# Optimization experiments

Measured on AMD Instinct MI355X. Metric: run time of the kernel, lower is better.

Reference implementation:

```python
import jax, jax.numpy as jnp
import numpy as np

B, S, D = 64, 2048, 64  # (batch*heads, seq_len, head_dim)

def setup_inputs() -> dict:
    key = jax.random.key(0)
    kq, kk, kv = jax.random.split(key, 3)
    q = jax.random.normal(kq, (B, S, D), dtype=jnp.float32)
    k = jax.random.normal(kk, (B, S, D), dtype=jnp.float32)
    v = jax.random.normal(kv, (B, S, D), dtype=jnp.float32)
    return {"q": q, "k": k, "v": v}

def reference(q, k, v):
    # scores: [B, S, S] = q @ k^T (no scaling, matching the source module)
    scores = jnp.einsum('bqd,bkd->bqk', q, k)
    attn = jax.nn.softmax(scores, axis=-1)
    # dropout p=0.0 -> identity
    out = jnp.einsum('bqk,bkd->bqd', attn, v)
    return out
```

## Files before the change

### kernel.cpp

```cpp
#include <hip/hip_runtime.h>

typedef __attribute__((ext_vector_type(8))) __bf16 bf16x8;
typedef __attribute__((ext_vector_type(8))) _Float16 f16x8;
typedef __attribute__((ext_vector_type(4))) float f32x4;
typedef __attribute__((ext_vector_type(8))) unsigned short u16x8;
typedef __attribute__((ext_vector_type(2))) unsigned int u32x2;

#define SDIM 2048
#define DDIM 64
#define NBATCH 64
#define LOG2E 1.44269504088896340736f

#if __has_builtin(__builtin_amdgcn_exp2f)
#define EXP2F __builtin_amdgcn_exp2f
#else
#define EXP2F exp2f
#endif

__device__ inline unsigned short f2bf(float f) {
  unsigned u = __builtin_bit_cast(unsigned, f);
  u += 0x7fffu + ((u >> 16) & 1u);
  return (unsigned short)(u >> 16);
}
__device__ inline unsigned short f2h(float f) {
  return __builtin_bit_cast(unsigned short, (_Float16)f);
}

__device__ inline void gload_lds16(const void* g, void* l) {
  __builtin_amdgcn_global_load_lds(
      (const __attribute__((address_space(1))) unsigned int*)g,
      (__attribute__((address_space(3))) unsigned int*)l, 16, 0, 0);
}

__global__ __launch_bounds__(256) void prep_kernel(
    const float* __restrict__ k, const float* __restrict__ v,
    unsigned short* __restrict__ khf, unsigned short* __restrict__ vtb) {
  __shared__ float tile[64][65];
  const int b = blockIdx.x >> 5;
  const int s0 = (blockIdx.x & 31) * 64;
  const size_t base = ((size_t)b * SDIM + s0) * DDIM;

  {
    const float* src = k + base + threadIdx.x * 16;
    f32x4 a = *(const f32x4*)src;
    f32x4 b4 = *(const f32x4*)(src + 4);
    f32x4 c4 = *(const f32x4*)(src + 8);
    f32x4 d4 = *(const f32x4*)(src + 12);
    u16x8 o0, o1;
#pragma unroll
    for (int j = 0; j < 4; ++j) {
      o0[j] = f2h(a[j] * LOG2E);
      o0[4 + j] = f2h(b4[j] * LOG2E);
      o1[j] = f2h(c4[j] * LOG2E);
      o1[4 + j] = f2h(d4[j] * LOG2E);
    }
    unsigned short* dst = khf + base + threadIdx.x * 16;
    *(u16x8*)dst = o0;
    *(u16x8*)(dst + 8) = o1;
  }

  {
    int row = threadIdx.x >> 2;
    int c16 = (threadIdx.x & 3) * 16;
    const float* src = v + base + (size_t)row * DDIM + c16;
#pragma unroll
    for (int c = 0; c < 4; ++c) {
      f32x4 f = *(const f32x4*)(src + 4 * c);
      tile[row][c16 + 4 * c + 0] = f[0];
      tile[row][c16 + 4 * c + 1] = f[1];
      tile[row][c16 + 4 * c + 2] = f[2];
      tile[row][c16 + 4 * c + 3] = f[3];
    }
    __syncthreads();
    int d = threadIdx.x >> 2;
    int sc = (threadIdx.x & 3) * 16;
    u16x8 a, c;
#pragma unroll
    for (int j = 0; j < 8; ++j) a[j] = f2bf(tile[sc + j][d]);
#pragma unroll
    for (int j = 0; j < 8; ++j) c[j] = f2bf(tile[sc + 8 + j][d]);
    unsigned short* dst = vtb + ((size_t)b * DDIM + d) * SDIM + s0 + sc;
    *(u16x8*)dst = a;
    *(u16x8*)(dst + 8) = c;
  }
}

__global__ __launch_bounds__(256, 2) void attn_kernel(
    const float* __restrict__ q, const unsigned short* __restrict__ khf,
    const unsigned short* __restrict__ vt, float* __restrict__ out) {
  __shared__ __align__(16) unsigned short kv[2 * 16 * 512];
  __shared__ __align__(16) unsigned short pf[4 * 8 * 512];

  const int bid = blockIdx.x;
  const int b = (bid & 7) * 8 + (bid >> 6);
  const int qt = (bid >> 3) & 7;
  const int tid = threadIdx.x;
  const int w = tid >> 6;
  const int L = tid & 63;
  const int l15 = L & 15;
  const int l4 = L >> 4;

  const size_t boff = (size_t)b * (SDIM * DDIM);
  const int qg = qt * 256 + w * 64;

  f16x8 qb[4][2];
#pragma unroll
  for (int t = 0; t < 4; ++t)
#pragma unroll
    for (int c = 0; c < 2; ++c) {
      const float* src = q + boff + (size_t)(qg + t * 16 + l15) * DDIM + c * 32 + l4 * 8;
      f32x4 f0 = *(const f32x4*)(src);
      f32x4 f1 = *(const f32x4*)(src + 4);
      f16x8 h;
#pragma unroll
      for (int j = 0; j < 4; ++j) {
        h[j] = (_Float16)f0[j];
        h[4 + j] = (_Float16)f1[j];
      }
      qb[t][c] = h;
    }

  const int pwoff = (l15 + 16 * (l4 >> 1)) * 8 + 4 * (l4 & 1);
  unsigned short* pwave = pf + w * 4096;

  const unsigned short* gsrc[4];
  int gadv;
  if (w < 2) {
#pragma unroll
    for (int ff = 0; ff < 4; ++ff) {
      int f = w * 4 + ff;
      gsrc[ff] = khf + boff + (size_t)((f >> 1) * 16 + l15) * DDIM + (f & 1) * 32 + l4 * 8;
    }
    gadv = 64 * DDIM;
  } else {
#pragma unroll
    for (int ff = 0; ff < 4; ++ff) {
      int fg = (w - 2) * 4 + ff;
      gsrc[ff] = vt + boff + (size_t)((fg >> 1) * 16 + l15) * SDIM + (fg & 1) * 32 + l4 * 8;
    }
    gadv = 64;
  }
  const int fdbase = w * 4;

  f32x4 o[4][4];
  float lsum[4];
#pragma unroll
  for (int t = 0; t < 4; ++t) {
#pragma unroll
    for (int n = 0; n < 4; ++n) o[t][n] = (f32x4){0.f, 0.f, 0.f, 0.f};
    lsum[t] = 0.f;
  }

#pragma unroll
  for (int ff = 0; ff < 4; ++ff) gload_lds16(gsrc[ff], &kv[(fdbase + ff) * 512]);
#pragma unroll
  for (int ff = 0; ff < 4; ++ff) gsrc[ff] += gadv;

  for (int it = 0; it < SDIM / 64; ++it) {
    const int cur = it & 1;
    __syncthreads();
    if (it + 1 < SDIM / 64) {
#pragma unroll
      for (int ff = 0; ff < 4; ++ff)
        gload_lds16(gsrc[ff], &kv[(1 - cur) * 8192 + (fdbase + ff) * 512]);
#pragma unroll
      for (int ff = 0; ff < 4; ++ff) gsrc[ff] += gadv;
    }
    const unsigned short* kvc = &kv[cur * 8192];

#pragma unroll
    for (int nt = 0; nt < 4; ++nt) {
      f16x8 k0 = *(const f16x8*)&kvc[(nt * 2 + 0) * 512 + L * 8];
      f16x8 k1 = *(const f16x8*)&kvc[(nt * 2 + 1) * 512 + L * 8];
      const int pbase = (nt >> 1) * 512 + pwoff + (nt & 1) * 256;
#pragma unroll
      for (int t = 0; t < 4; ++t) {
        f32x4 acc = (f32x4){0.f, 0.f, 0.f, 0.f};
        acc = __builtin_amdgcn_mfma_f32_16x16x32_f16(k0, qb[t][0], acc, 0, 0, 0);
        acc = __builtin_amdgcn_mfma_f32_16x16x32_f16(k1, qb[t][1], acc, 0, 0, 0);
        float p0 = EXP2F(acc[0]), p1 = EXP2F(acc[1]);
        float p2 = EXP2F(acc[2]), p3 = EXP2F(acc[3]);
        lsum[t] += (p0 + p1) + (p2 + p3);
        unsigned a0 = __builtin_bit_cast(unsigned, p0) + 0x8000u;
        unsigned a1 = __builtin_bit_cast(unsigned, p1) + 0x8000u;
        unsigned a2 = __builtin_bit_cast(unsigned, p2) + 0x8000u;
        unsigned a3 = __builtin_bit_cast(unsigned, p3) + 0x8000u;
        u32x2 wv;
        wv[0] = __builtin_amdgcn_perm(a1, a0, 0x07060302u);
        wv[1] = __builtin_amdgcn_perm(a3, a2, 0x07060302u);
        *(u32x2*)&pwave[t * 1024 + pbase] = wv;
      }
    }

    bf16x8 vv[8];
#pragma unroll
    for (int i = 0; i < 8; ++i) vv[i] = *(const bf16x8*)&kvc[(8 + i) * 512 + L * 8];
#pragma unroll
    for (int t = 0; t < 4; ++t) {
      bf16x8 p0 = *(const bf16x8*)&pwave[(t * 2 + 0) * 512 + L * 8];
      bf16x8 p1 = *(const bf16x8*)&pwave[(t * 2 + 1) * 512 + L * 8];
#pragma unroll
      for (int n = 0; n < 4; ++n) {
        o[t][n] = __builtin_amdgcn_mfma_f32_16x16x32_bf16(p0, vv[n * 2 + 0], o[t][n], 0, 0, 0);
        o[t][n] = __builtin_amdgcn_mfma_f32_16x16x32_bf16(p1, vv[n * 2 + 1], o[t][n], 0, 0, 0);
      }
    }
  }

#pragma unroll
  for (int t = 0; t < 4; ++t) {
    lsum[t] += __shfl_xor(lsum[t], 16);
    lsum[t] += __shfl_xor(lsum[t], 32);
  }
#pragma unroll
  for (int t = 0; t < 4; ++t) {
    float rc[4];
#pragma unroll
    for (int r = 0; r < 4; ++r) rc[r] = 1.f / __shfl(lsum[t], l4 * 4 + r);
#pragma unroll
    for (int n = 0; n < 4; ++n)
#pragma unroll
      for (int r = 0; r < 4; ++r)
        out[boff + (size_t)(qg + t * 16 + l4 * 4 + r) * DDIM + n * 16 + l15] =
            o[t][n][r] * rc[r];
  }
}

extern "C" void kernel_launch(void* const* d_in, const int* in_sizes, int n_in,
                              void* d_out, int out_size, void* d_ws, size_t ws_size,
                              hipStream_t stream) {
  const float* q = (const float*)d_in[0];
  const float* k = (const float*)d_in[1];
  const float* v = (const float*)d_in[2];
  float* out = (float*)d_out;
  unsigned short* khf = (unsigned short*)d_ws;
  unsigned short* vt = khf + (size_t)NBATCH * SDIM * DDIM;

  prep_kernel<<<NBATCH * (SDIM / 64), 256, 0, stream>>>(k, v, khf, vt);
  attn_kernel<<<NBATCH * (SDIM / 256), 256, 0, stream>>>(q, khf, vt, out);
}
```

Before: 215.1 us.

## Keep softmax probabilities in registers by permuting K rows to match MFMA layout

Reorders K rows when loading into LDS so that the QK^T MFMA accumulator layout of two 16-key tiles directly forms the A-operand fragment for the PV MFMA. This removes the per-wave LDS buffer for P, including the write, barrier-free re-read and its 32KB of shared memory. It also replaces the manual round-and-perm bf16 packing with the hardware v_cvt_pk_bf16_f32 instruction. The trade-off is a more intricate key-index permutation that must stay consistent with the V^T k-ordering, and some extra register pressure from holding the V fragments alongside the scores.

```diff
diff --git a/kernel.cpp b/kernel.cpp
--- a/kernel.cpp
+++ b/kernel.cpp
@@ -4,7 +4,7 @@
 typedef __attribute__((ext_vector_type(8))) _Float16 f16x8;
 typedef __attribute__((ext_vector_type(4))) float f32x4;
 typedef __attribute__((ext_vector_type(8))) unsigned short u16x8;
-typedef __attribute__((ext_vector_type(2))) unsigned int u32x2;
+typedef __attribute__((ext_vector_type(4))) unsigned int u32x4;
 
 #define SDIM 2048
 #define DDIM 64
@@ -24,6 +24,11 @@
 }
 __device__ inline unsigned short f2h(float f) {
   return __builtin_bit_cast(unsigned short, (_Float16)f);
+}
+__device__ inline unsigned cvtpk_bf16(float lo, float hi) {
+  unsigned r;
+  asm("v_cvt_pk_bf16_f32 %0, %1, %2" : "=v"(r) : "v"(lo), "v"(hi));
+  return r;
 }
 
 __device__ inline void gload_lds16(const void* g, void* l) {
@@ -89,7 +94,6 @@
     const float* __restrict__ q, const unsigned short* __restrict__ khf,
     const unsigned short* __restrict__ vt, float* __restrict__ out) {
   __shared__ __align__(16) unsigned short kv[2 * 16 * 512];
-  __shared__ __align__(16) unsigned short pf[4 * 8 * 512];
 
   const int bid = blockIdx.x;
   const int b = (bid & 7) * 8 + (bid >> 6);
@@ -120,16 +124,14 @@
       qb[t][c] = h;
     }
 
-  const int pwoff = (l15 + 16 * (l4 >> 1)) * 8 + 4 * (l4 & 1);
-  unsigned short* pwave = pf + w * 4096;
-
   const unsigned short* gsrc[4];
   int gadv;
   if (w < 2) {
 #pragma unroll
     for (int ff = 0; ff < 4; ++ff) {
       int f = w * 4 + ff;
-      gsrc[ff] = khf + boff + (size_t)((f >> 1) * 16 + l15) * DDIM + (f & 1) * 32 + l4 * 8;
+      int srow = 32 * (f >> 2) + 8 * (l15 >> 2) + 4 * ((f >> 1) & 1) + (l15 & 3);
+      gsrc[ff] = khf + boff + (size_t)srow * DDIM + (f & 1) * 32 + l4 * 8;
     }
     gadv = 64 * DDIM;
   } else {
@@ -169,40 +171,35 @@
     const unsigned short* kvc = &kv[cur * 8192];
 
 #pragma unroll
-    for (int nt = 0; nt < 4; ++nt) {
-      f16x8 k0 = *(const f16x8*)&kvc[(nt * 2 + 0) * 512 + L * 8];
-      f16x8 k1 = *(const f16x8*)&kvc[(nt * 2 + 1) * 512 + L * 8];
-      const int pbase = (nt >> 1) * 512 + pwoff + (nt & 1) * 256;
+    for (int c = 0; c < 2; ++c) {
+      f16x8 ka0 = *(const f16x8*)&kvc[(4 * c + 0) * 512 + L * 8];
+      f16x8 ka1 = *(const f16x8*)&kvc[(4 * c + 1) * 512 + L * 8];
+      f16x8 kb0 = *(const f16x8*)&kvc[(4 * c + 2) * 512 + L * 8];
+      f16x8 kb1 = *(const f16x8*)&kvc[(4 * c + 3) * 512 + L * 8];
+      bf16x8 vcr[4];
+#pragma unroll
+      for (int n = 0; n < 4; ++n) vcr[n] = *(const bf16x8*)&kvc[(8 + 2 * n + c) * 512 + L * 8];
+
 #pragma unroll
       for (int t = 0; t < 4; ++t) {
-        f32x4 acc = (f32x4){0.f, 0.f, 0.f, 0.f};
-        acc = __builtin_amdgcn_mfma_f32_16x16x32_f16(k0, qb[t][0], acc, 0, 0, 0);
-        acc = __builtin_amdgcn_mfma_f32_16x16x32_f16(k1, qb[t][1], acc, 0, 0, 0);
-        float p0 = EXP2F(acc[0]), p1 = EXP2F(acc[1]);
-        float p2 = EXP2F(acc[2]), p3 = EXP2F(acc[3]);
-        lsum[t] += (p0 + p1) + (p2 + p3);
-        unsigned a0 = __builtin_bit_cast(unsigned, p0) + 0x8000u;
-        unsigned a1 = __builtin_bit_cast(unsigned, p1) + 0x8000u;
-        unsigned a2 = __builtin_bit_cast(unsigned, p2) + 0x8000u;
-        unsigned a3 = __builtin_bit_cast(unsigned, p3) + 0x8000u;
-        u32x2 wv;
-        wv[0] = __builtin_amdgcn_perm(a1, a0, 0x07060302u);
-        wv[1] = __builtin_amdgcn_perm(a3, a2, 0x07060302u);
-        *(u32x2*)&pwave[t * 1024 + pbase] = wv;
-      }
-    }
-
-    bf16x8 vv[8];
-#pragma unroll
-    for (int i = 0; i < 8; ++i) vv[i] = *(const bf16x8*)&kvc[(8 + i) * 512 + L * 8];
-#pragma unroll
-    for (int t = 0; t < 4; ++t) {
-      bf16x8 p0 = *(const bf16x8*)&pwave[(t * 2 + 0) * 512 + L * 8];
-      bf16x8 p1 = *(const bf16x8*)&pwave[(t * 2 + 1) * 512 + L * 8];
-#pragma unroll
-      for (int n = 0; n < 4; ++n) {
-        o[t][n] = __builtin_amdgcn_mfma_f32_16x16x32_bf16(p0, vv[n * 2 + 0], o[t][n], 0, 0, 0);
-        o[t][n] = __builtin_amdgcn_mfma_f32_16x16x32_bf16(p1, vv[n * 2 + 1], o[t][n], 0, 0, 0);
+        f32x4 aT0 = (f32x4){0.f, 0.f, 0.f, 0.f};
+        f32x4 aT1 = (f32x4){0.f, 0.f, 0.f, 0.f};
+        aT0 = __builtin_amdgcn_mfma_f32_16x16x32_f16(ka0, qb[t][0], aT0, 0, 0, 0);
+        aT0 = __builtin_amdgcn_mfma_f32_16x16x32_f16(ka1, qb[t][1], aT0, 0, 0, 0);
+        aT1 = __builtin_amdgcn_mfma_f32_16x16x32_f16(kb0, qb[t][0], aT1, 0, 0, 0);
+        aT1 = __builtin_amdgcn_mfma_f32_16x16x32_f16(kb1, qb[t][1], aT1, 0, 0, 0);
+        float p0 = EXP2F(aT0[0]), p1 = EXP2F(aT0[1]), p2 = EXP2F(aT0[2]), p3 = EXP2F(aT0[3]);
+        float p4 = EXP2F(aT1[0]), p5 = EXP2F(aT1[1]), p6 = EXP2F(aT1[2]), p7 = EXP2F(aT1[3]);
+        lsum[t] += ((p0 + p1) + (p2 + p3)) + ((p4 + p5) + (p6 + p7));
+        u32x4 pw;
+        pw[0] = cvtpk_bf16(p0, p1);
+        pw[1] = cvtpk_bf16(p2, p3);
+        pw[2] = cvtpk_bf16(p4, p5);
+        pw[3] = cvtpk_bf16(p6, p7);
+        bf16x8 pfrag = __builtin_bit_cast(bf16x8, pw);
+#pragma unroll
+        for (int n = 0; n < 4; ++n)
+          o[t][n] = __builtin_amdgcn_mfma_f32_16x16x32_bf16(pfrag, vcr[n], o[t][n], 0, 0, 0);
       }
     }
   }
```

Result: faster. 198.9 us (-7.5%).
